# Performance work log

Measured on AMD Instinct MI355X. Metric: run time of the kernel, lower is better.

## Reference

```python
import jax, jax.numpy as jnp
import numpy as np

NUM_HEADS = 8
WINDOW = 5
DILATION = 1


def _offsets(window, dilation):
    r = dilation * (window // 2)
    return [(dy, dx) for dy in range(-r, r + 1, dilation)
            for dx in range(-r, r + 1, dilation)]


def _neighbors(x, window, dilation):
    # x: [B, heads, head_dim, Hc, Wc] -> [B, heads, K, head_dim, Hc, Wc]
    B, Hn, hd, Hc, Wc = x.shape
    r = dilation * (window // 2)
    xp = jnp.pad(x, ((0, 0), (0, 0), (0, 0), (r, r), (r, r)))
    offs = _offsets(window, dilation)
    return jnp.stack(
        [xp[..., r + dy:r + dy + Hc, r + dx:r + dx + Wc] for dy, dx in offs],
        axis=2)


def _valid_mask(Hc, Wc, window, dilation):
    # [K, Hc, Wc] bool: True where the shifted neighbor lies inside the map
    ys = jnp.arange(Hc)
    xs = jnp.arange(Wc)
    offs = _offsets(window, dilation)
    return jnp.stack(
        [(((ys + dy) >= 0) & ((ys + dy) < Hc))[:, None]
         & (((xs + dx) >= 0) & ((xs + dx) < Wc))[None, :]
         for dy, dx in offs], axis=0)


def _align_to_query_grid(t, out_h, out_w, scale):
    # repeat coarse lattice onto the fine query grid via anchor indexing
    y = jnp.clip(jnp.arange(out_h) // scale, 0, t.shape[-2] - 1)
    x = jnp.clip(jnp.arange(out_w) // scale, 0, t.shape[-1] - 1)
    return jnp.take(jnp.take(t, y, axis=-2), x, axis=-1)


def setup_inputs() -> dict:
    key = jax.random.key(0)
    k1, k2 = jax.random.split(key)
    k = jax.random.normal(k1, (2, 128, 48, 48), dtype=jnp.float32)
    v = jax.random.normal(k2, (2, 128, 48, 48), dtype=jnp.float32)
    return {"k": k, "v": v, "query_height": 96, "query_width": 96,
            "scale_factor": 2}


def reference(k, v, query_height, query_width, scale_factor):
    B, C, Hc, Wc = k.shape
    hd = C // NUM_HEADS
    kh = k.reshape(B, NUM_HEADS, hd, Hc, Wc)
    vh = v.reshape(B, NUM_HEADS, hd, Hc, Wc)
    k_nb = _neighbors(kh, WINDOW, DILATION)  # [B,H,K,hd,Hc,Wc]
    v_nb = _neighbors(vh, WINDOW, DILATION)
    mask = _valid_mask(Hc, Wc, WINDOW, DILATION)  # [K,Hc,Wc]
    K = mask.shape[0]
    mask = jnp.broadcast_to(mask[None, None], (B, NUM_HEADS, K, Hc, Wc))
    k_nb = _align_to_query_grid(k_nb, query_height, query_width, scale_factor)
    v_nb = _align_to_query_grid(v_nb, query_height, query_width, scale_factor)
    mask = _align_to_query_grid(mask, query_height, query_width, scale_factor)
    return (k_nb, v_nb, mask)
```

## Files before the change

### kernel.cpp

```cpp
#include <hip/hip_runtime.h>


#define KV_ELEMS  58982400LL
#define MASK_OFF  117964800LL

__global__ __launch_bounds__(256) void kv_expand_kernel(
    const float* __restrict__ k, const float* __restrict__ v,
    float* __restrict__ out_k, float* __restrict__ out_v) {
    int tid = blockIdx.x * blockDim.x + threadIdx.x;
    int x4 = tid % 24;  int t = tid / 24;
    int y  = t % 96;    t /= 96;
    int d  = t % 16;    t /= 16;
    int kk = t % 25;    t /= 25;
    int h  = t % 8;
    int b  = t / 8;

    int dy = kk / 5 - 2;
    int dx = kk % 5 - 2;
    int yy = (y >> 1) + dy;
    bool vy = (unsigned)yy < 48u;
    int xc0 = 2 * x4 + dx;
    int xc1 = xc0 + 1;
    bool v0 = vy && ((unsigned)xc0 < 48u);
    bool v1 = vy && ((unsigned)xc1 < 48u);

    int base = ((b * 128 + h * 16 + d) * 48 + (vy ? yy : 0)) * 48;
    float k0 = v0 ? k[base + xc0] : 0.0f;
    float k1 = v1 ? k[base + xc1] : 0.0f;
    float w0 = v0 ? v[base + xc0] : 0.0f;
    float w1 = v1 ? v[base + xc1] : 0.0f;

    float4 ok = make_float4(k0, k0, k1, k1);
    float4 ov = make_float4(w0, w0, w1, w1);
    reinterpret_cast<float4*>(out_k)[tid] = ok;
    reinterpret_cast<float4*>(out_v)[tid] = ov;
}

__global__ __launch_bounds__(256) void mask_kernel(float* __restrict__ out_m) {
    int tid = blockIdx.x * blockDim.x + threadIdx.x;
    int x4 = tid % 24;  int t = tid / 24;
    int y  = t % 96;    t /= 96;
    int kk = t % 25;

    int dy = kk / 5 - 2;
    int dx = kk % 5 - 2;
    int yy = (y >> 1) + dy;
    bool vy = (unsigned)yy < 48u;
    int xc0 = 2 * x4 + dx;
    bool v0 = vy && ((unsigned)xc0 < 48u);
    bool v1 = vy && ((unsigned)(xc0 + 1) < 48u);

    float m0 = v0 ? 1.0f : 0.0f;
    float m1 = v1 ? 1.0f : 0.0f;
    reinterpret_cast<float4*>(out_m)[tid] = make_float4(m0, m0, m1, m1);
}

extern "C" void kernel_launch(void* const* d_in, const int* in_sizes, int n_in,
                              void* d_out, int out_size, void* d_ws, size_t ws_size,
                              hipStream_t stream) {
    const float* k = (const float*)d_in[0];
    const float* v = (const float*)d_in[1];
    float* out = (float*)d_out;
    float* out_k = out;
    float* out_v = out + KV_ELEMS;
    float* out_m = out + MASK_OFF;

    kv_expand_kernel<<<57600, 256, 0, stream>>>(k, v, out_k, out_v);
    mask_kernel<<<3600, 256, 0, stream>>>(out_m);
}
```

Baseline: 478.7 us.

## Fuse mask into KV expand kernel with 3D grid and nontemporal stores

Merges the mask kernel into the KV expansion kernel, so the first 9 blocks of each (batch*head, window offset) slice also write the mask for that slice. Switches to a 3D grid, which removes most of the per-thread div/mod index decoding. Loads become unconditional from clamped addresses, with zeros selected afterward. Outputs are written with nontemporal stores, since the workload is a write-bound broadcast of about 470 MB; the change also saves one kernel launch.

```diff
diff --git a/kernel.cpp b/kernel.cpp
--- a/kernel.cpp
+++ b/kernel.cpp
@@ -4,55 +4,60 @@
 #define KV_ELEMS  58982400LL
 #define MASK_OFF  117964800LL
 
-__global__ __launch_bounds__(256) void kv_expand_kernel(
+typedef float f32x4 __attribute__((ext_vector_type(4)));
+
+__global__ __launch_bounds__(256) void fused_expand_kernel(
     const float* __restrict__ k, const float* __restrict__ v,
-    float* __restrict__ out_k, float* __restrict__ out_v) {
-    int tid = blockIdx.x * blockDim.x + threadIdx.x;
-    int x4 = tid % 24;  int t = tid / 24;
-    int y  = t % 96;    t /= 96;
-    int d  = t % 16;    t /= 16;
-    int kk = t % 25;    t /= 25;
-    int h  = t % 8;
-    int b  = t / 8;
+    float* __restrict__ out_k, float* __restrict__ out_v,
+    float* __restrict__ out_m) {
+    const int t  = blockIdx.x * 256 + threadIdx.x;
+    const int kk = blockIdx.y;
+    const int z  = blockIdx.z;
 
-    int dy = kk / 5 - 2;
-    int dx = kk % 5 - 2;
-    int yy = (y >> 1) + dy;
-    bool vy = (unsigned)yy < 48u;
-    int xc0 = 2 * x4 + dx;
-    int xc1 = xc0 + 1;
-    bool v0 = vy && ((unsigned)xc0 < 48u);
-    bool v1 = vy && ((unsigned)xc1 < 48u);
+    const int q  = t / 24;
+    const int x4 = t - q * 24;
+    const int d  = q / 96;
+    const int y  = q - d * 96;
 
-    int base = ((b * 128 + h * 16 + d) * 48 + (vy ? yy : 0)) * 48;
-    float k0 = v0 ? k[base + xc0] : 0.0f;
-    float k1 = v1 ? k[base + xc1] : 0.0f;
-    float w0 = v0 ? v[base + xc0] : 0.0f;
-    float w1 = v1 ? v[base + xc1] : 0.0f;
+    const int kq = kk / 5;
+    const int dy = kq - 2;
+    const int dx = kk - kq * 5 - 2;
 
-    float4 ok = make_float4(k0, k0, k1, k1);
-    float4 ov = make_float4(w0, w0, w1, w1);
-    reinterpret_cast<float4*>(out_k)[tid] = ok;
-    reinterpret_cast<float4*>(out_v)[tid] = ov;
-}
+    const int yy  = (y >> 1) + dy;
+    const bool vy = (unsigned)yy < 48u;
+    const int xc0 = 2 * x4 + dx;
+    const int xc1 = xc0 + 1;
+    const bool v0 = vy && ((unsigned)xc0 < 48u);
+    const bool v1 = vy && ((unsigned)xc1 < 48u);
 
-__global__ __launch_bounds__(256) void mask_kernel(float* __restrict__ out_m) {
-    int tid = blockIdx.x * blockDim.x + threadIdx.x;
-    int x4 = tid % 24;  int t = tid / 24;
-    int y  = t % 96;    t /= 96;
-    int kk = t % 25;
+    const int yc = vy ? yy : 0;
+    const int x0 = min(max(xc0, 0), 47);
+    const int x1 = min(max(xc1, 0), 47);
 
-    int dy = kk / 5 - 2;
-    int dx = kk % 5 - 2;
-    int yy = (y >> 1) + dy;
-    bool vy = (unsigned)yy < 48u;
-    int xc0 = 2 * x4 + dx;
-    bool v0 = vy && ((unsigned)xc0 < 48u);
-    bool v1 = vy && ((unsigned)(xc0 + 1) < 48u);
+    const int base = ((z * 16 + d) * 48 + yc) * 48;
+    float k0 = k[base + x0];
+    float k1 = k[base + x1];
+    float w0 = v[base + x0];
+    float w1 = v[base + x1];
+    k0 = v0 ? k0 : 0.0f;
+    k1 = v1 ? k1 : 0.0f;
+    w0 = v0 ? w0 : 0.0f;
+    w1 = v1 ? w1 : 0.0f;
 
-    float m0 = v0 ? 1.0f : 0.0f;
-    float m1 = v1 ? 1.0f : 0.0f;
-    reinterpret_cast<float4*>(out_m)[tid] = make_float4(m0, m0, m1, m1);
+    const int slice = z * 25 + kk;
+    const int o = slice * 36864 + t;
+    f32x4 ok = {k0, k0, k1, k1};
+    f32x4 ov = {w0, w0, w1, w1};
+    __builtin_nontemporal_store(ok, reinterpret_cast<f32x4*>(out_k) + o);
+    __builtin_nontemporal_store(ov, reinterpret_cast<f32x4*>(out_v) + o);
+
+    if (blockIdx.x < 9) {
+        const float m0 = v0 ? 1.0f : 0.0f;
+        const float m1 = v1 ? 1.0f : 0.0f;
+        f32x4 om = {m0, m0, m1, m1};
+        __builtin_nontemporal_store(
+            om, reinterpret_cast<f32x4*>(out_m) + slice * 2304 + t);
+    }
 }
 
 extern "C" void kernel_launch(void* const* d_in, const int* in_sizes, int n_in,
@@ -65,6 +70,6 @@
     float* out_v = out + KV_ELEMS;
     float* out_m = out + MASK_OFF;
 
-    kv_expand_kernel<<<57600, 256, 0, stream>>>(k, v, out_k, out_v);
-    mask_kernel<<<3600, 256, 0, stream>>>(out_m);
+    fused_expand_kernel<<<dim3(144, 25, 16), 256, 0, stream>>>(
+        k, v, out_k, out_v, out_m);
 }
```

After: 468.2 us. 2.2% less time.
